# Optimization experiments

Hardware: AMD Instinct MI355X
Metric: run time of the kernel (lower is better)

Reference implementation:

```python
import jax, jax.numpy as jnp
import numpy as np

DIM = 2048
N_EXPERTS = 16
TOP_K = 4
MOE_INTER = 1024
SHARED_INTER = 2 * MOE_INTER  # n_shared_experts * moe_inter_dim
B, S = 4, 1024
INIT = 0.02


def setup_inputs() -> dict:
    key = jax.random.key(0)
    ks = jax.random.split(key, 8)
    return {
        "x": jax.random.normal(ks[0], (B, S, DIM), dtype=jnp.float32),
        "gate_w": jax.random.normal(ks[1], (DIM, N_EXPERTS), dtype=jnp.float32) * INIT,
        "w1": jax.random.normal(ks[2], (N_EXPERTS, DIM, MOE_INTER), dtype=jnp.float32) * INIT,
        "w2": jax.random.normal(ks[3], (N_EXPERTS, MOE_INTER, DIM), dtype=jnp.float32) * INIT,
        "w3": jax.random.normal(ks[4], (N_EXPERTS, DIM, MOE_INTER), dtype=jnp.float32) * INIT,
        "ws1": jax.random.normal(ks[5], (DIM, SHARED_INTER), dtype=jnp.float32) * INIT,
        "ws2": jax.random.normal(ks[6], (SHARED_INTER, DIM), dtype=jnp.float32) * INIT,
        "ws3": jax.random.normal(ks[7], (DIM, SHARED_INTER), dtype=jnp.float32) * INIT,
    }


def _moe_forward(x, gate_w, w1, w2, w3, ws1, ws2, ws3):
    shape = x.shape
    xf = x.reshape(-1, DIM)  # [T, D]
    # Gate: softmax scores, top-k selection (weights are the top-k probs)
    scores = jax.nn.softmax(xf @ gate_w, axis=-1)          # [T, E]
    weights, indices = jax.lax.top_k(scores, TOP_K)         # [T, K] each
    y = jnp.zeros_like(xf)
    # Fixed loop over experts (structural, not over data dims).
    for e in range(N_EXPERTS):
        # gate coefficient for expert e: 0 if not in token's top-k
        coef = jnp.sum(weights * (indices == e), axis=-1)   # [T]
        h = jax.nn.silu(xf @ w1[e]) * (xf @ w3[e])          # [T, I]
        y = y + coef[:, None] * (h @ w2[e])
    # Shared experts (always-on gated MLP)
    z = (jax.nn.silu(xf @ ws1) * (xf @ ws3)) @ ws2
    return (y + z).reshape(shape)


def reference(x, gate_w, w1, w2, w3, ws1, ws2, ws3):
    return _moe_forward(x, gate_w, w1, w2, w3, ws1, ws2, ws3)
```

## Files before the change

kernel.cpp:

```cpp
#include <hip/hip_runtime.h>
#include <hip/hip_bf16.h>
#include <stdint.h>

#define T_TOK 4096
#define DIMD  2048
#define NEXP  16
#define TOPK  4
#define NI    1024
#define NSH   2048

typedef __attribute__((ext_vector_type(8))) short short8;
typedef __attribute__((ext_vector_type(4))) float f32x4;
typedef __attribute__((ext_vector_type(4))) unsigned short u16x4;
typedef __attribute__((ext_vector_type(8))) unsigned short u16x8;

__device__ __forceinline__ unsigned short f2bf(float f) {
    union { float f; unsigned u; } v; v.f = f;
    return (unsigned short)((v.u + 0x7fffu + ((v.u >> 16) & 1u)) >> 16);
}

__device__ __forceinline__ void gload16(const void* g, void* l) {
    __builtin_amdgcn_global_load_lds(
        (const __attribute__((address_space(1))) void*)g,
        (__attribute__((address_space(3))) void*)l, 16, 0, 0);
}

__global__ __launch_bounds__(256) void gwt_kernel(const float* __restrict__ gw,
                                                  float* __restrict__ gwT) {
    int i = blockIdx.x * 256 + threadIdx.x;
    int d = i >> 4, e = i & 15;
    gwT[e * DIMD + d] = gw[i];
}

__global__ __launch_bounds__(256) void gate_kernel(const float* __restrict__ x,
                                                   const float* __restrict__ gwT,
                                                   int* __restrict__ blk_cnt,
                                                   int* __restrict__ tk_er,
                                                   float* __restrict__ tk_wv) {
    __shared__ int h[16];
    const int blk = blockIdx.x;
    const int t = blk * 4 + (threadIdx.x >> 6);
    const int lane = threadIdx.x & 63;
    if (threadIdx.x < 16) h[threadIdx.x] = 0;
    __syncthreads();

    const f32x4* xr = (const f32x4*)(x + (size_t)t * DIMD);
    f32x4 xv[8];
#pragma unroll
    for (int i = 0; i < 8; ++i) xv[i] = xr[i * 64 + lane];

    float acc[NEXP];
#pragma unroll
    for (int e = 0; e < NEXP; ++e) {
        const f32x4* gr = (const f32x4*)(gwT + e * DIMD);
        float s = 0.f;
#pragma unroll
        for (int i = 0; i < 8; ++i) {
            f32x4 gv = gr[i * 64 + lane];
            s += xv[i][0] * gv[0] + xv[i][1] * gv[1] +
                 xv[i][2] * gv[2] + xv[i][3] * gv[3];
        }
        acc[e] = s;
    }
#pragma unroll
    for (int e = 0; e < NEXP; ++e) {
        float v = acc[e];
#pragma unroll
        for (int off = 32; off; off >>= 1) v += __shfl_xor(v, off, 64);
        acc[e] = v;
    }
    float m = acc[0];
#pragma unroll
    for (int e = 1; e < NEXP; ++e) m = fmaxf(m, acc[e]);
    float s = 0.f;
#pragma unroll
    for (int e = 0; e < NEXP; ++e) { acc[e] = expf(acc[e] - m); s += acc[e]; }
    float inv = 1.f / s;
#pragma unroll
    for (int e = 0; e < NEXP; ++e) acc[e] *= inv;

    float w4[TOPK]; int i4[TOPK];
#pragma unroll
    for (int k = 0; k < TOPK; ++k) {
        float bv = -1.f; int be = 0;
#pragma unroll
        for (int e = 0; e < NEXP; ++e)
            if (acc[e] > bv) { bv = acc[e]; be = e; }
        w4[k] = bv; i4[k] = be;
#pragma unroll
        for (int e = 0; e < NEXP; ++e)
            if (e == be) acc[e] = -1.f;
    }

    if (lane == 0) {
        int r4[TOPK];
#pragma unroll
        for (int k = 0; k < TOPK; ++k) r4[k] = atomicAdd(&h[i4[k]], 1);
#pragma unroll
        for (int k = 0; k < TOPK; ++k) {
            tk_er[t * 4 + k] = (i4[k] << 20) | r4[k];
            tk_wv[t * 4 + k] = w4[k];
        }
    }
    __syncthreads();
    if (threadIdx.x < 16) blk_cnt[blk * 16 + threadIdx.x] = h[threadIdx.x];
}

__global__ __launch_bounds__(256) void scan_kernel(const int* __restrict__ blk_cnt,
                                                   int* __restrict__ blk_off,
                                                   int* __restrict__ cnt,
                                                   int* __restrict__ offs,
                                                   int* __restrict__ table) {
    __shared__ int gsum[16][17];
    __shared__ int gbase[16][17];
    __shared__ int csh[16];
    int tid = threadIdx.x;
    int e = tid >> 4, g = tid & 15;
    {
        int s = 0;
        for (int b = g * 64; b < g * 64 + 64; ++b) s += blk_cnt[b * 16 + e];
        gsum[e][g] = s;
    }
    __syncthreads();
    if (tid < 16) {
        int run = 0;
        for (int g2 = 0; g2 < 16; ++g2) { gbase[tid][g2] = run; run += gsum[tid][g2]; }
        csh[tid] = run;
        cnt[tid] = run;
    }
    __syncthreads();
    {
        int run = gbase[e][g];
        for (int b = g * 64; b < g * 64 + 64; ++b) {
            blk_off[b * 16 + e] = run;
            run += blk_cnt[b * 16 + e];
        }
    }
    if (tid == 0) {
        int o = 0;
        for (int e2 = 0; e2 < 16; ++e2) { offs[e2] = o; o += csh[e2]; }
        offs[NEXP] = o;
        int ns = 0;
        for (int e2 = 0; e2 < 16; ++e2)
            for (int rb = 0; rb < csh[e2]; rb += 128) {
                table[ns] = (e2 << 16) | rb; ++ns;
            }
        table[255] = ns;
    }
}

__global__ __launch_bounds__(256) void fill_kernel(const int* __restrict__ tk_er,
                                                   const float* __restrict__ tk_wv,
                                                   const int* __restrict__ blk_off,
                                                   int* __restrict__ list,
                                                   float* __restrict__ cw) {
    int i = blockIdx.x * 256 + threadIdx.x;
    int rec = tk_er[i];
    int e = rec >> 20, r = rec & 0xFFFFF;
    int t = i >> 2;
    int ro = blk_off[(t >> 2) * 16 + e] + r;
    list[e * T_TOK + ro] = t;
    cw[e * T_TOK + ro] = tk_wv[i];
}

__global__ __launch_bounds__(256) void cvt_kernel(const float* __restrict__ x,
                                                  unsigned short* __restrict__ xb) {
    int i = blockIdx.x * 256 + threadIdx.x;
    const f32x4* src = (const f32x4*)x;
    f32x4 a = src[i * 2 + 0];
    f32x4 b = src[i * 2 + 1];
    short8 o;
#pragma unroll
    for (int j = 0; j < 4; ++j) o[j] = (short)f2bf(a[j]);
#pragma unroll
    for (int j = 0; j < 4; ++j) o[4 + j] = (short)f2bf(b[j]);
    ((short8*)xb)[i] = o;
}

__global__ __launch_bounds__(256) void tq_pair(const float* __restrict__ s1,
                                               const float* __restrict__ s3,
                                               unsigned short* __restrict__ dst,
                                               int K, int N,
                                               size_t srcStrideE, size_t dstStrideE) {
    int e = blockIdx.z;
    s1 += (size_t)e * srcStrideE;
    s3 += (size_t)e * srcStrideE;
    dst += (size_t)e * dstStrideE;
    __shared__ unsigned short tile[64][72];
    const int t = threadIdx.x;
    const int k0 = blockIdx.y * 64, n0 = blockIdx.x * 64;
    const int lr = t >> 4, lc4 = (t & 15) * 4;
    const int sr8 = (t & 7) * 8, sn = t >> 3;
#pragma unroll
    for (int half = 0; half < 2; ++half) {
        const float* src = half ? s3 : s1;
#pragma unroll
        for (int r = 0; r < 4; ++r) {
            f32x4 v = *(const f32x4*)(src + (size_t)(k0 + lr + r * 16) * N + n0 + lc4);
#pragma unroll
            for (int j = 0; j < 4; ++j) tile[lr + r * 16][lc4 + j] = f2bf(v[j]);
        }
        __syncthreads();
#pragma unroll
        for (int q = 0; q < 2; ++q) {
            int nn = sn + q * 32;
            int n = n0 + nn;
            int rrow = (n >> 4) * 32 + half * 16 + (n & 15);
            u16x8 o;
#pragma unroll
            for (int j = 0; j < 8; ++j) o[j] = tile[sr8 + j][nn];
            *(u16x8*)(dst + (size_t)rrow * K + k0 + sr8) = o;
        }
        __syncthreads();
    }
}

__global__ __launch_bounds__(256) void tq_plain(const float* __restrict__ src,
                                                unsigned short* __restrict__ dst,
                                                int K, int N,
                                                size_t srcStrideE, size_t dstStrideE) {
    int e = blockIdx.z;
    src += (size_t)e * srcStrideE;
    dst += (size_t)e * dstStrideE;
    __shared__ unsigned short tile[64][72];
    const int t = threadIdx.x;
    const int k0 = blockIdx.y * 64, n0 = blockIdx.x * 64;
    const int lr = t >> 4, lc4 = (t & 15) * 4;
    const int sr8 = (t & 7) * 8, sn = t >> 3;
#pragma unroll
    for (int r = 0; r < 4; ++r) {
        f32x4 v = *(const f32x4*)(src + (size_t)(k0 + lr + r * 16) * N + n0 + lc4);
#pragma unroll
        for (int j = 0; j < 4; ++j) tile[lr + r * 16][lc4 + j] = f2bf(v[j]);
    }
    __syncthreads();
#pragma unroll
    for (int q = 0; q < 2; ++q) {
        int nn = sn + q * 32;
        int n = n0 + nn;
        u16x8 o;
#pragma unroll
        for (int j = 0; j < 8; ++j) o[j] = tile[sr8 + j][nn];
        *(u16x8*)(dst + (size_t)n * K + k0 + sr8) = o;
    }
}

template <bool UP>
__global__ __launch_bounds__(512, 2) void gemm_f(
    const unsigned short* __restrict__ Ash, const unsigned short* __restrict__ Art,
    const unsigned short* __restrict__ Bsh, const unsigned short* __restrict__ Brt,
    const int* __restrict__ cnt, const int* __restrict__ offs,
    const int* __restrict__ list, const float* __restrict__ cw,
    unsigned short* __restrict__ hs, unsigned short* __restrict__ hbuf,
    float* __restrict__ fout, const int* __restrict__ table) {
    constexpr int NT = UP ? 64 : 32;

    const int bid = blockIdx.x;
    const bool routed = bid >= 512;
    int bx, rb, e = 0, M, obase = 0, kb = 0;
    const unsigned short* Ap;
    const unsigned short* Bp;
    int ASTRr, BSTRr;
    if (!routed) {
        if (UP) { bx = bid & 15; rb = (bid >> 4) * 128; }
        else    { bx = bid & 7;  rb = ((bid >> 3) & 31) * 128; kb = (bid >> 8) * 1024; }
        M = T_TOK;
        Ap = Ash; Bp = Bsh;
        ASTRr = 2048; BSTRr = 2048;
    } else {
        int rbid = bid - 512;
        int slot = rbid >> 3;
        if (slot >= table[255]) return;
        bx = rbid & 7;
        int pk = table[slot];
        e = pk >> 16; rb = pk & 0xFFFF;
        M = cnt[e]; obase = offs[e];
        Ap = Art;
        Bp = Brt + (UP ? (size_t)e * 2048 * 2048 : (size_t)e * 2048 * 1024);
        ASTRr = UP ? 2048 : 1024;
        BSTRr = UP ? 2048 : 1024;
    }

    extern __shared__ char smem[];

    const int tid = threadIdx.x;
    const int lane = tid & 63, wid = tid >> 6;
    const int wm = wid >> 2, wn = wid & 3;
    const int fr = lane & 15, fq = lane >> 4;
    const int offR = ((fr >> 1) << 7) + (((((fr & 1) << 2) | fq) ^ (fr >> 1)) << 4);
    const int d16 = tid * 16;

    const unsigned short* pA;
    const unsigned short* pB0;
    const unsigned short* pB1;
    {
        int c = tid, s = c >> 3, sl = (c & 7) ^ (s & 7);
        int rA = 2 * s + (sl >> 2), kk = (sl & 3) * 8;
        int gr = rb + rA;
        int cr = (gr < M) ? gr : (M - 1);
        size_t arow;
        if (!routed)  arow = (size_t)gr;
        else if (UP)  arow = (size_t)list[e * T_TOK + cr];
        else          arow = (size_t)(obase + cr);
        pA = Ap + arow * ASTRr + kb + kk;
    }
#pragma unroll
    for (int u = 0; u < 2; ++u) {
        int c = u * 512 + tid, s = c >> 3, sl = (c & 7) ^ (s & 7);
        int rB = 2 * s + (sl >> 2), kk = (sl & 3) * 8;
        const unsigned short* p = Bp + (size_t)(bx * 256 + rB) * BSTRr + kb + kk;
        if (u == 0) pB0 = p; else pB1 = p;
    }

    f32x4 acc[4][4];
#pragma unroll
    for (int m = 0; m < 4; ++m)
#pragma unroll
        for (int n = 0; n < 4; ++n) acc[m][n] = (f32x4)0.f;

    gload16(pA,      (void*)(smem + 0 + d16));
    gload16(pA + 32, (void*)(smem + 8192 + d16));
    gload16(pB0,      (void*)(smem + 24576 + d16));
    gload16(pB1,      (void*)(smem + 24576 + 8192 + d16));
    gload16(pB0 + 32, (void*)(smem + 24576 + 16384 + d16));
    gload16(pB1 + 32, (void*)(smem + 24576 + 16384 + 8192 + d16));
    pA += 64; pB0 += 64; pB1 += 64;
    asm volatile("s_waitcnt vmcnt(0)" ::: "memory");
    __builtin_amdgcn_s_barrier();

    int bA = 0, bA2 = 16384;
    int bB = 0, bB2 = 32768;
    for (int t = 0; t < NT; ++t) {
        short8 aF[4], bF[4];
#pragma unroll
        for (int m = 0; m < 4; ++m)
            aF[m] = *(const short8*)(smem + bA + wm * 4096 + m * 1024 + offR);
#pragma unroll
        for (int n = 0; n < 4; ++n)
            bF[n] = *(const short8*)(smem + 24576 + bB + wn * 4096 + n * 1024 + offR);
        const bool more = (t + 2 < NT);
        if (more) {
            gload16(pA, (void*)(smem + bA2 + d16));
            gload16(pB0, (void*)(smem + 24576 + bB2 + d16));
            gload16(pB1, (void*)(smem + 24576 + bB2 + 8192 + d16));
            pA += 32; pB0 += 32; pB1 += 32;
        }
        __builtin_amdgcn_s_setprio(1);
#pragma unroll
        for (int m = 0; m < 4; ++m)
#pragma unroll
            for (int n = 0; n < 4; ++n)
                acc[m][n] = __builtin_amdgcn_mfma_f32_16x16x32_bf16(aF[m], bF[n], acc[m][n], 0, 0, 0);
        __builtin_amdgcn_s_setprio(0);
        if (more) { asm volatile("s_waitcnt vmcnt(3)" ::: "memory"); }
        else      { asm volatile("s_waitcnt vmcnt(0)" ::: "memory"); }
        __builtin_amdgcn_s_barrier();
        bA = (bA == 16384) ? 0 : bA + 8192;
        bA2 = (bA2 == 16384) ? 0 : bA2 + 8192;
        bB = (bB == 32768) ? 0 : bB + 16384;
        bB2 = (bB2 == 32768) ? 0 : bB2 + 16384;
    }

    if constexpr (UP) {
        const int LDO = routed ? NI : NSH;
        unsigned short* hp = routed ? hbuf : hs;
#pragma unroll
        for (int m = 0; m < 4; ++m)
#pragma unroll
            for (int q = 0; q < 4; ++q) {
                int gr = rb + wm * 64 + m * 16 + fq * 4 + q;
                if (gr < M) {
                    float coef = routed ? cw[e * T_TOK + gr] : 1.f;
                    size_t orow = (size_t)((routed ? obase : 0) + gr) * LDO;
#pragma unroll
                    for (int nfp = 0; nfp < 2; ++nfp) {
                        float c1 = acc[m][2 * nfp][q], c3 = acc[m][2 * nfp + 1][q];
                        float h = c1 / (1.f + __expf(-c1)) * c3 * coef;
                        int ncol = (bx * 8 + wn * 2 + nfp) * 16 + fr;
                        hp[orow + ncol] = f2bf(h);
                    }
                }
            }
    } else {
#pragma unroll
        for (int m = 0; m < 4; ++m)
#pragma unroll
            for (int q = 0; q < 4; ++q) {
                int gr = rb + wm * 64 + m * 16 + fq * 4 + q;
                if (gr < M) {
                    int orow = routed ? list[e * T_TOK + gr] : gr;
#pragma unroll
                    for (int nf = 0; nf < 4; ++nf) {
                        int col = bx * 256 + wn * 64 + nf * 16 + fr;
                        atomicAdd(fout + (size_t)orow * DIMD + col, acc[m][nf][q]);
                    }
                }
            }
    }
}

extern "C" void kernel_launch(void* const* d_in, const int* in_sizes, int n_in,
                              void* d_out, int out_size, void* d_ws, size_t ws_size,
                              hipStream_t stream) {
    const float* x   = (const float*)d_in[0];
    const float* gw  = (const float*)d_in[1];
    const float* w1  = (const float*)d_in[2];
    const float* w2  = (const float*)d_in[3];
    const float* w3  = (const float*)d_in[4];
    const float* ws1 = (const float*)d_in[5];
    const float* ws2 = (const float*)d_in[6];
    const float* ws3 = (const float*)d_in[7];
    float* out = (float*)d_out;

    char* p = (char*)d_ws;
    unsigned short* xb   = (unsigned short*)p; p += (size_t)T_TOK * DIMD * 2;
    unsigned short* hs   = (unsigned short*)p; p += (size_t)T_TOK * NSH * 2;
    unsigned short* hbuf = (unsigned short*)p; p += (size_t)T_TOK * TOPK * NI * 2;
    unsigned short* upT  = (unsigned short*)p; p += (size_t)NEXP * 2048 * DIMD * 2;
    unsigned short* w2T  = (unsigned short*)p; p += (size_t)NEXP * DIMD * NI * 2;
    unsigned short* upsT = (unsigned short*)p; p += (size_t)2 * NSH * DIMD * 2;
    unsigned short* ws2T = (unsigned short*)p; p += (size_t)DIMD * NSH * 2;
    float* gwT = (float*)p;                    p += (size_t)NEXP * DIMD * 4;
    float* cw = (float*)p;                     p += (size_t)NEXP * T_TOK * 4;
    int* list = (int*)p;                       p += (size_t)NEXP * T_TOK * 4;
    int* tk_er = (int*)p;                      p += (size_t)T_TOK * TOPK * 4;
    float* tk_wv = (float*)p;                  p += (size_t)T_TOK * TOPK * 4;
    int* blk_cnt = (int*)p;                    p += (size_t)1024 * 16 * 4;
    int* blk_off = (int*)p;                    p += (size_t)1024 * 16 * 4;
    int* cnt = (int*)p;                        p += 256;
    int* offs = (int*)p;                       p += 256;
    int* table = (int*)p;                      p += 1024;
    if ((size_t)(p - (char*)d_ws) > ws_size) return;

    hipFuncSetAttribute((const void*)&gemm_f<true>, hipFuncAttributeMaxDynamicSharedMemorySize, 73728);
    hipFuncSetAttribute((const void*)&gemm_f<false>, hipFuncAttributeMaxDynamicSharedMemorySize, 73728);

    hipMemsetAsync(out, 0, (size_t)out_size * 4, stream);
    gwt_kernel<<<(NEXP * DIMD) / 256, 256, 0, stream>>>(gw, gwT);
    gate_kernel<<<T_TOK / 4, 256, 0, stream>>>(x, gwT, blk_cnt, tk_er, tk_wv);
    scan_kernel<<<1, 256, 0, stream>>>(blk_cnt, blk_off, cnt, offs, table);
    fill_kernel<<<T_TOK * TOPK / 256, 256, 0, stream>>>(tk_er, tk_wv, blk_off, list, cw);
    cvt_kernel<<<(T_TOK * DIMD / 8) / 256, 256, 0, stream>>>(x, xb);

    tq_pair<<<dim3(NI / 64, DIMD / 64, NEXP), 256, 0, stream>>>(
        w1, w3, upT, DIMD, NI, (size_t)DIMD * NI, (size_t)2048 * DIMD);
    tq_pair<<<dim3(NSH / 64, DIMD / 64, 1), 256, 0, stream>>>(
        ws1, ws3, upsT, DIMD, NSH, 0, 0);
    tq_plain<<<dim3(DIMD / 64, NI / 64, NEXP), 256, 0, stream>>>(
        w2, w2T, NI, DIMD, (size_t)NI * DIMD, (size_t)DIMD * NI);
    tq_plain<<<dim3(DIMD / 64, NSH / 64, 1), 256, 0, stream>>>(
        ws2, ws2T, NSH, DIMD, 0, 0);

    gemm_f<true><<<512 + 144 * 8, 512, 73728, stream>>>(
        xb, xb, upsT, upT, cnt, offs, list, cw, hs, hbuf, nullptr, table);
    gemm_f<false><<<512 + 144 * 8, 512, 73728, stream>>>(
        hs, hbuf, ws2T, w2T, cnt, offs, list, nullptr, nullptr, nullptr, out, table);
}
```

Baseline: 663.9 us.

## Replace down-proj atomics with plain stores and a per-token gather reduction

The down-projection GEMM no longer uses atomicAdd into the output. The shared expert now runs over the full K=2048 without split-K and writes the output directly. Routed experts write per-slot rows into a scratch buffer that aliases the transposed up-weights, and a new gather kernel sums each token's four expert rows into the output. This removes the output memset and the atomic contention. In exchange it adds an extra fp32 write and read of about 64 MB and gives the shared down-proj GEMM fewer blocks.

Result: faster. 627.5 us (-5.5%).

```diff
diff --git a/kernel.cpp b/kernel.cpp
--- a/kernel.cpp
+++ b/kernel.cpp
@@ -152,8 +152,10 @@
 __global__ __launch_bounds__(256) void fill_kernel(const int* __restrict__ tk_er,
                                                    const float* __restrict__ tk_wv,
                                                    const int* __restrict__ blk_off,
+                                                   const int* __restrict__ offs,
                                                    int* __restrict__ list,
-                                                   float* __restrict__ cw) {
+                                                   float* __restrict__ cw,
+                                                   int* __restrict__ rows) {
     int i = blockIdx.x * 256 + threadIdx.x;
     int rec = tk_er[i];
     int e = rec >> 20, r = rec & 0xFFFFF;
@@ -161,6 +163,7 @@
     int ro = blk_off[(t >> 2) * 16 + e] + r;
     list[e * T_TOK + ro] = t;
     cw[e * T_TOK + ro] = tk_wv[i];
+    rows[i] = offs[e] + ro;
 }
 
 __global__ __launch_bounds__(256) void cvt_kernel(const float* __restrict__ x,
@@ -245,6 +248,30 @@
     }
 }
 
+__global__ __launch_bounds__(256) void gather_kernel(const float* __restrict__ dbuf,
+                                                     const int* __restrict__ rows,
+                                                     float* __restrict__ out) {
+    const int t = blockIdx.x;
+    const int c8 = threadIdx.x * 8;
+    int r[4];
+#pragma unroll
+    for (int k = 0; k < 4; ++k) r[k] = rows[t * 4 + k];
+    f32x4 a0, a1;
+    {
+        const f32x4* z = (const f32x4*)(out + (size_t)t * DIMD + c8);
+        a0 = z[0]; a1 = z[1];
+    }
+#pragma unroll
+    for (int k = 0; k < 4; ++k) {
+        const f32x4* d = (const f32x4*)(dbuf + (size_t)r[k] * DIMD + c8);
+        f32x4 d0 = d[0], d1 = d[1];
+#pragma unroll
+        for (int j = 0; j < 4; ++j) { a0[j] += d0[j]; a1[j] += d1[j]; }
+    }
+    f32x4* o = (f32x4*)(out + (size_t)t * DIMD + c8);
+    o[0] = a0; o[1] = a1;
+}
+
 template <bool UP>
 __global__ __launch_bounds__(512, 2) void gemm_f(
     const unsigned short* __restrict__ Ash, const unsigned short* __restrict__ Art,
@@ -252,23 +279,24 @@
     const int* __restrict__ cnt, const int* __restrict__ offs,
     const int* __restrict__ list, const float* __restrict__ cw,
     unsigned short* __restrict__ hs, unsigned short* __restrict__ hbuf,
-    float* __restrict__ fout, const int* __restrict__ table) {
-    constexpr int NT = UP ? 64 : 32;
+    float* __restrict__ fout, float* __restrict__ dbuf,
+    const int* __restrict__ table) {
+    constexpr int SHBLK = UP ? 512 : 256;
 
     const int bid = blockIdx.x;
-    const bool routed = bid >= 512;
-    int bx, rb, e = 0, M, obase = 0, kb = 0;
+    const bool routed = bid >= SHBLK;
+    int bx, rb, e = 0, M, obase = 0;
     const unsigned short* Ap;
     const unsigned short* Bp;
     int ASTRr, BSTRr;
     if (!routed) {
         if (UP) { bx = bid & 15; rb = (bid >> 4) * 128; }
-        else    { bx = bid & 7;  rb = ((bid >> 3) & 31) * 128; kb = (bid >> 8) * 1024; }
+        else    { bx = bid & 7;  rb = (bid >> 3) * 128; }
         M = T_TOK;
         Ap = Ash; Bp = Bsh;
         ASTRr = 2048; BSTRr = 2048;
     } else {
-        int rbid = bid - 512;
+        int rbid = bid - SHBLK;
         int slot = rbid >> 3;
         if (slot >= table[255]) return;
         bx = rbid & 7;
@@ -280,6 +308,7 @@
         ASTRr = UP ? 2048 : 1024;
         BSTRr = UP ? 2048 : 1024;
     }
+    const int NT = (!UP && routed) ? 32 : 64;
 
     extern __shared__ char smem[];
 
@@ -302,13 +331,13 @@
         if (!routed)  arow = (size_t)gr;
         else if (UP)  arow = (size_t)list[e * T_TOK + cr];
         else          arow = (size_t)(obase + cr);
-        pA = Ap + arow * ASTRr + kb + kk;
+        pA = Ap + arow * ASTRr + kk;
     }
 #pragma unroll
     for (int u = 0; u < 2; ++u) {
         int c = u * 512 + tid, s = c >> 3, sl = (c & 7) ^ (s & 7);
         int rB = 2 * s + (sl >> 2), kk = (sl & 3) * 8;
-        const unsigned short* p = Bp + (size_t)(bx * 256 + rB) * BSTRr + kb + kk;
+        const unsigned short* p = Bp + (size_t)(bx * 256 + rB) * BSTRr + kk;
         if (u == 0) pB0 = p; else pB1 = p;
     }
 
@@ -388,11 +417,12 @@
             for (int q = 0; q < 4; ++q) {
                 int gr = rb + wm * 64 + m * 16 + fq * 4 + q;
                 if (gr < M) {
-                    int orow = routed ? list[e * T_TOK + gr] : gr;
+                    float* op = routed ? (dbuf + (size_t)(obase + gr) * DIMD)
+                                       : (fout + (size_t)gr * DIMD);
 #pragma unroll
                     for (int nf = 0; nf < 4; ++nf) {
                         int col = bx * 256 + wn * 64 + nf * 16 + fr;
-                        atomicAdd(fout + (size_t)orow * DIMD + col, acc[m][nf][q]);
+                        op[col] = acc[m][nf][q];
                     }
                 }
             }
@@ -425,21 +455,23 @@
     int* list = (int*)p;                       p += (size_t)NEXP * T_TOK * 4;
     int* tk_er = (int*)p;                      p += (size_t)T_TOK * TOPK * 4;
     float* tk_wv = (float*)p;                  p += (size_t)T_TOK * TOPK * 4;
+    int* rows = (int*)p;                       p += (size_t)T_TOK * TOPK * 4;
     int* blk_cnt = (int*)p;                    p += (size_t)1024 * 16 * 4;
     int* blk_off = (int*)p;                    p += (size_t)1024 * 16 * 4;
     int* cnt = (int*)p;                        p += 256;
     int* offs = (int*)p;                       p += 256;
     int* table = (int*)p;                      p += 1024;
     if ((size_t)(p - (char*)d_ws) > ws_size) return;
+    float* dbuf = (float*)upT;
 
     hipFuncSetAttribute((const void*)&gemm_f<true>, hipFuncAttributeMaxDynamicSharedMemorySize, 73728);
     hipFuncSetAttribute((const void*)&gemm_f<false>, hipFuncAttributeMaxDynamicSharedMemorySize, 73728);
 
-    hipMemsetAsync(out, 0, (size_t)out_size * 4, stream);
     gwt_kernel<<<(NEXP * DIMD) / 256, 256, 0, stream>>>(gw, gwT);
     gate_kernel<<<T_TOK / 4, 256, 0, stream>>>(x, gwT, blk_cnt, tk_er, tk_wv);
     scan_kernel<<<1, 256, 0, stream>>>(blk_cnt, blk_off, cnt, offs, table);
-    fill_kernel<<<T_TOK * TOPK / 256, 256, 0, stream>>>(tk_er, tk_wv, blk_off, list, cw);
+    fill_kernel<<<T_TOK * TOPK / 256, 256, 0, stream>>>(tk_er, tk_wv, blk_off, offs,
+                                                        list, cw, rows);
     cvt_kernel<<<(T_TOK * DIMD / 8) / 256, 256, 0, stream>>>(x, xb);
 
     tq_pair<<<dim3(NI / 64, DIMD / 64, NEXP), 256, 0, stream>>>(
@@ -452,7 +484,8 @@
         ws2, ws2T, NSH, DIMD, 0, 0);
 
     gemm_f<true><<<512 + 144 * 8, 512, 73728, stream>>>(
-        xb, xb, upsT, upT, cnt, offs, list, cw, hs, hbuf, nullptr, table);
-    gemm_f<false><<<512 + 144 * 8, 512, 73728, stream>>>(
-        hs, hbuf, ws2T, w2T, cnt, offs, list, nullptr, nullptr, nullptr, out, table);
-}
+        xb, xb, upsT, upT, cnt, offs, list, cw, hs, hbuf, nullptr, nullptr, table);
+    gemm_f<false><<<256 + 144 * 8, 512, 73728, stream>>>(
+        hs, hbuf, ws2T, w2T, cnt, offs, list, nullptr, nullptr, nullptr, out, dbuf, table);
+    gather_kernel<<<T_TOK, 256, 0, stream>>>(dbuf, rows, out);
+}
```
